# Kernel optimization log

Hardware: AMD Instinct MI355X
Metric: run time of the kernel (lower is better)

Reference implementation:

```python
import jax, jax.numpy as jnp
import numpy as np

N = 8  # fixed node count per sample (hardcoded in the torch module)


def setup_inputs() -> dict:
    key = jax.random.key(0)
    ks = jax.random.split(key, 13)
    B = 131072

    def w(k, shape, fan_in):
        # torch nn.Linear default init: U(-1/sqrt(fan_in), 1/sqrt(fan_in))
        return jax.random.uniform(k, shape, jnp.float32, -1.0, 1.0) / np.sqrt(fan_in).astype(np.float32)

    return {
        "x": jax.random.normal(ks[0], (B, N), jnp.float32),
        "enc_w1": w(ks[1], (3, 64), 3),   "enc_b1": w(ks[2], (64,), 3),
        "enc_w2": w(ks[3], (64, 2), 64),  "enc_b2": w(ks[4], (2,), 64),
        "gcn1_w": w(ks[5], (2, 32), 2),   "gcn1_b": w(ks[6], (32,), 2),
        "gcn2_w": w(ks[7], (32, 32), 32), "gcn2_b": w(ks[8], (32,), 32),
        "dec_w1": w(ks[9], (32, 64), 32), "dec_b1": w(ks[10], (64,), 32),
        "dec_w2": w(ks[11], (64, 3), 64), "dec_b2": w(ks[12], (3,), 64),
    }


def _gabriel_norm_adj(p):
    """Batched Gabriel graph -> GCN-normalized (A + I) with unit edge weights.

    p: (B, N, 2) latent 2D points.
    Edge (i,j) exists iff no other point k lies strictly inside the circle
    with diameter (p_i, p_j)  (dist(p_k, mid)^2 < r^2, matching torch's '<').
    Gabriel graphs contain the nearest-neighbor graph, so for N>=2 edges always
    exist and the torch fallback branch is unreachable.
    Returns D^{-1/2} (A + I) D^{-1/2} of shape (B, N, N) (GCNConv default:
    add_self_loops=True with weight 1, symmetric normalization).
    """
    mid = (p[:, :, None, :] + p[:, None, :, :]) * 0.5                 # (B,N,N,2)
    r2 = jnp.sum((p[:, :, None, :] - mid) ** 2, axis=-1)              # (B,N,N)
    # d2[b,i,j,k] = ||p[b,k] - mid[b,i,j]||^2  -> (B,N,N,N), the big intermediate
    d2 = jnp.sum((p[:, None, None, :, :] - mid[:, :, :, None, :]) ** 2, axis=-1)
    a = jnp.arange(N)
    k_not_ij = (a[None, None, :] != a[:, None, None]) & (a[None, None, :] != a[None, :, None])  # (N,N,N) [i,j,k]
    blocked = jnp.any((d2 < r2[..., None]) & k_not_ij, axis=-1)       # (B,N,N)
    off_diag = a[:, None] != a[None, :]
    adj = ((~blocked) & off_diag).astype(p.dtype)                     # symmetric Gabriel adjacency
    a_hat = adj + jnp.eye(N, dtype=p.dtype)                           # self-loops, weight 1
    dinv = jax.lax.rsqrt(jnp.sum(a_hat, axis=-1))                     # (B,N)
    return dinv[:, :, None] * a_hat * dinv[:, None, :]


def reference(x, enc_w1, enc_b1, enc_w2, enc_b2,
              gcn1_w, gcn1_b, gcn2_w, gcn2_b,
              dec_w1, dec_b1, dec_w2, dec_b2):
    B = x.shape[0]
    idx = jnp.arange(N, dtype=x.dtype)
    # preprocess: (B, N, 3) rows [0, value, index]
    xp = jnp.stack([jnp.zeros_like(x), x, jnp.broadcast_to(idx, x.shape)], axis=-1)
    latent = jax.nn.relu(xp @ enc_w1 + enc_b1) @ enc_w2 + enc_b2      # (B,N,2)
    # torch builds the graph from detach().cpu().numpy() -> no grad through structure
    norm = jax.lax.stop_gradient(_gabriel_norm_adj(latent))           # (B,N,N)
    h1 = jax.nn.relu(jnp.einsum('bij,bjf->bif', norm, latent @ gcn1_w) + gcn1_b)  # (B,N,32)
    h2 = jnp.einsum('bij,bjf->bif', norm, h1 @ gcn2_w) + gcn2_b                    # (B,N,32)
    pooled = jnp.mean(h2, axis=1)                                     # (B,32)
    node = jnp.broadcast_to(pooled[:, None, :], (B, N, pooled.shape[-1]))
    dec = jax.nn.relu(node @ dec_w1 + dec_b1) @ dec_w2 + dec_b2       # (B,N,3)
    reconstructed = dec[:, :, 1]                                      # (B,N)
    return reconstructed, latent
```

## Files before the change

### kernel.cpp

```cpp
#include <hip/hip_runtime.h>


typedef float v2 __attribute__((ext_vector_type(2)));
static __device__ __forceinline__ v2 sp(float s) { return (v2){s, s}; }
static __device__ __forceinline__ v2 fma2(v2 a, v2 b, v2 c) {
    return __builtin_elementwise_fma(a, b, c);
}
static __device__ __forceinline__ v2 ldv2(const float* p) {
    return *reinterpret_cast<const v2*>(p);
}

__global__ __launch_bounds__(256) void gae_aux(
    const float* __restrict__ gcn2_w, const float* __restrict__ gcn2_b,
    const float* __restrict__ dec_w1, const float* __restrict__ dec_b1,
    const float* __restrict__ dec_w2, float* __restrict__ ws)
{
    const int tid = blockIdx.x * 256 + threadIdx.x;
    const int f = tid >> 6, h = tid & 63;
    float acc = 0.0f;
    #pragma unroll 8
    for (int g = 0; g < 32; ++g)
        acc = fmaf(gcn2_w[f * 32 + g], dec_w1[g * 64 + h], acc);
    ws[f * 64 + h] = acc;
    if (tid < 64) {
        float c = dec_b1[h];
        #pragma unroll 8
        for (int g = 0; g < 32; ++g)
            c = fmaf(gcn2_b[g], dec_w1[g * 64 + h], c);
        ws[2048 + h] = c;
        ws[2112 + h] = dec_w2[h * 3 + 1];
    }
}

__global__ __launch_bounds__(256, 4) void gae_main(
    const float* __restrict__ x,
    const float* __restrict__ enc_w1,
    const float* __restrict__ enc_b1,
    const float* __restrict__ enc_w2,
    const float* __restrict__ enc_b2,
    const float* __restrict__ gcn1_w,
    const float* __restrict__ gcn1_b,
    const float* __restrict__ ws,
    const float* __restrict__ dec_b2,
    float* __restrict__ out_rec,
    float* __restrict__ out_lat,
    int B)
{
    __shared__ v2    pbuf[2][8][64];
    __shared__ v2    tbuf[2][16][64];
    __shared__ float obuf[2][2][64];

    const int lane = threadIdx.x & 63;
    const int wid  = threadIdx.x >> 6;
    const int wp   = wid >> 1;
    const int ru   = __builtin_amdgcn_readfirstlane(wid & 1);
    int g = blockIdx.x * 128 + wp * 64 + lane;
    if (g >= B) g = B - 1;

    const float4 xr = *reinterpret_cast<const float4*>(x + (size_t)g * 8 + 4 * ru);
    const v2 xA = (v2){xr.x, xr.y};
    const v2 xB = (v2){xr.z, xr.w};
    const float i0 = (float)(4 * ru);
    const v2 ipA = (v2){i0, i0 + 1.0f};
    const v2 ipB = (v2){i0 + 2.0f, i0 + 3.0f};

    v2 pl0, pl1, pl2, pl3;
    {
        const v2 b2v = ldv2(enc_b2);
        pl0 = b2v; pl1 = b2v; pl2 = b2v; pl3 = b2v;
    }
    #pragma unroll 4
    for (int h = 0; h < 64; ++h) {
        const float wx = enc_w1[64 + h];
        const float wi = enc_w1[128 + h];
        const float bb = enc_b1[h];
        const v2 uxy = ldv2(enc_w2 + 2 * h);
        v2 cA = fma2(ipA, sp(wi), sp(bb));
        v2 cB = fma2(ipB, sp(wi), sp(bb));
        v2 tA = fma2(xA, sp(wx), cA);
        v2 tB = fma2(xB, sp(wx), cB);
        tA = __builtin_elementwise_max(tA, sp(0.0f));
        tB = __builtin_elementwise_max(tB, sp(0.0f));
        pl0 = fma2(sp(tA.x), uxy, pl0);
        pl1 = fma2(sp(tA.y), uxy, pl1);
        pl2 = fma2(sp(tB.x), uxy, pl2);
        pl3 = fma2(sp(tB.y), uxy, pl3);
    }

    {
        float4* lo = reinterpret_cast<float4*>(out_lat + (size_t)g * 16 + 8 * ru);
        lo[0] = make_float4(pl0.x, pl0.y, pl1.x, pl1.y);
        lo[1] = make_float4(pl2.x, pl2.y, pl3.x, pl3.y);
    }

    pbuf[wp][4 * ru + 0][lane] = pl0;
    pbuf[wp][4 * ru + 1][lane] = pl1;
    pbuf[wp][4 * ru + 2][lane] = pl2;
    pbuf[wp][4 * ru + 3][lane] = pl3;
    __syncthreads();
    v2 p[8];
    #pragma unroll
    for (int j = 0; j < 8; ++j) p[j] = pbuf[wp][j][lane];

    unsigned m[8];
    #pragma unroll
    for (int i = 0; i < 8; ++i) m[i] = 1u << i;
    {
        #pragma clang fp contract(off)
        #pragma unroll
        for (int i = 0; i < 8; ++i) {
            #pragma unroll
            for (int j = i + 1; j < 8; ++j) {
                v2 mid = (p[i] + p[j]) * sp(0.5f);
                v2 di = p[i] - mid;  v2 si = di * di;  float r2i = si.x + si.y;
                v2 dj = p[j] - mid;  v2 sj = dj * dj;  float r2j = sj.x + sj.y;
                float dmin = 3.4e38f;
                #pragma unroll
                for (int k = 0; k < 8; ++k) {
                    if (k == i || k == j) continue;
                    v2 dk = p[k] - mid;
                    v2 sk = dk * dk;
                    dmin = fminf(dmin, sk.x + sk.y);
                }
                m[i] |= (dmin < r2i) ? 0u : (1u << j);
                m[j] |= (dmin < r2j) ? 0u : (1u << i);
            }
        }
    }

    float dinv[8];
    #pragma unroll
    for (int i = 0; i < 8; ++i)
        dinv[i] = __builtin_amdgcn_rsqf((float)__popc(m[i]));

    v2 q[8];
    #pragma unroll
    for (int j = 0; j < 8; ++j) q[j] = sp(dinv[j]) * p[j];

    v2 n[8];
    #pragma unroll
    for (int i = 0; i < 8; ++i) {
        v2 acc = sp(0.0f);
        #pragma unroll
        for (int j = 0; j < 8; ++j)
            acc = fma2(sp((float)((m[i] >> j) & 1u)), q[j], acc);
        n[i] = sp(dinv[i]) * acc;
    }

    float cj[8];
    #pragma unroll
    for (int j = 0; j < 8; ++j) {
        float s = 0.0f;
        #pragma unroll
        for (int i = 0; i < 8; ++i)
            s = fmaf((float)((m[i] >> j) & 1u), dinv[i], s);
        cj[j] = 0.125f * dinv[j] * s;
    }

    const float* w0 = gcn1_w + 16 * ru;
    const float* w1 = gcn1_w + 32 + 16 * ru;
    const float* bl = gcn1_b + 16 * ru;
    v2 t2[8];
    #pragma unroll
    for (int fp = 0; fp < 8; ++fp) t2[fp] = sp(0.0f);
    #pragma unroll
    for (int i = 0; i < 8; ++i) {
        const v2 nxi = sp(n[i].x), nyi = sp(n[i].y), ci = sp(cj[i]);
        #pragma unroll
        for (int fp = 0; fp < 8; ++fp) {
            v2 h = fma2(nxi, ldv2(w0 + 2 * fp),
                   fma2(nyi, ldv2(w1 + 2 * fp), ldv2(bl + 2 * fp)));
            h = __builtin_elementwise_max(h, sp(0.0f));
            t2[fp] = fma2(ci, h, t2[fp]);
        }
    }

    #pragma unroll
    for (int fp = 0; fp < 8; ++fp) tbuf[wp][8 * ru + fp][lane] = t2[fp];
    __syncthreads();
    v2 tf[16];
    #pragma unroll
    for (int fp = 0; fp < 16; ++fp) tf[fp] = tbuf[wp][fp][lane];

    const float* Wd = ws + 32 * ru;
    const float* cd = ws + 2048 + 32 * ru;
    const float* w2 = ws + 2112 + 32 * ru;
    v2 a2[16];
    #pragma unroll
    for (int hp = 0; hp < 16; ++hp) a2[hp] = ldv2(cd + 2 * hp);
    #pragma unroll
    for (int f = 0; f < 32; ++f) {
        const v2 pf = sp(tf[f >> 1][f & 1]);
        const float* wr = Wd + f * 64;
        #pragma unroll
        for (int hp = 0; hp < 16; ++hp)
            a2[hp] = fma2(pf, ldv2(wr + 2 * hp), a2[hp]);
    }
    v2 oacc = sp(0.0f);
    #pragma unroll
    for (int hp = 0; hp < 16; ++hp) {
        v2 rr = __builtin_elementwise_max(a2[hp], sp(0.0f));
        oacc = fma2(rr, ldv2(w2 + 2 * hp), oacc);
    }
    const float opart = oacc.x + oacc.y;

    obuf[wp][ru][lane] = opart;
    __syncthreads();
    const float outv = (opart + obuf[wp][1 - ru][lane]) + dec_b2[1];

    {
        float4 r4 = make_float4(outv, outv, outv, outv);
        *reinterpret_cast<float4*>(out_rec + (size_t)g * 8 + 4 * ru) = r4;
    }
}

extern "C" void kernel_launch(void* const* d_in, const int* in_sizes, int n_in,
                              void* d_out, int out_size, void* d_ws, size_t ws_size,
                              hipStream_t stream) {
    const float* x       = (const float*)d_in[0];
    const float* enc_w1  = (const float*)d_in[1];
    const float* enc_b1  = (const float*)d_in[2];
    const float* enc_w2  = (const float*)d_in[3];
    const float* enc_b2  = (const float*)d_in[4];
    const float* gcn1_w  = (const float*)d_in[5];
    const float* gcn1_b  = (const float*)d_in[6];
    const float* gcn2_w  = (const float*)d_in[7];
    const float* gcn2_b  = (const float*)d_in[8];
    const float* dec_w1  = (const float*)d_in[9];
    const float* dec_b1  = (const float*)d_in[10];
    const float* dec_w2  = (const float*)d_in[11];
    const float* dec_b2  = (const float*)d_in[12];

    const int B = in_sizes[0] / 8;
    float* out_rec = (float*)d_out;
    float* out_lat = out_rec + (size_t)B * 8;
    float* ws      = (float*)d_ws;

    gae_aux<<<8, 256, 0, stream>>>(gcn2_w, gcn2_b, dec_w1, dec_b1, dec_w2, ws);

    const int threads = 256;
    const int blocks  = (2 * B + threads - 1) / threads;
    gae_main<<<blocks, threads, 0, stream>>>(
        x, enc_w1, enc_b1, enc_w2, enc_b2,
        gcn1_w, gcn1_b, ws, dec_b2,
        out_rec, out_lat, B);
}
```

Measured before the change: 113.7 us.

## Split each sample across four wavefronts instead of two, sharing graph work

Each sample is now handled by four threads (one per wavefront) instead of two. The 28 Gabriel pair tests are split 7 per wavefront and the adjacency bits are merged through shared memory. The aggregation, GCN and decoder stages are likewise split four ways using shared buffers, and the encoder's index-times-weight-plus-bias term is precomputed into a table by the aux kernel. This cuts per-thread work and register use, allowing 8 waves per SIMD, at the cost of extra barriers and shared-memory traffic.

```diff
diff --git a/kernel.cpp b/kernel.cpp
--- a/kernel.cpp
+++ b/kernel.cpp
@@ -13,7 +13,8 @@
 __global__ __launch_bounds__(256) void gae_aux(
     const float* __restrict__ gcn2_w, const float* __restrict__ gcn2_b,
     const float* __restrict__ dec_w1, const float* __restrict__ dec_b1,
-    const float* __restrict__ dec_w2, float* __restrict__ ws)
+    const float* __restrict__ dec_w2, const float* __restrict__ enc_w1,
+    const float* __restrict__ enc_b1, float* __restrict__ ws)
 {
     const int tid = blockIdx.x * 256 + threadIdx.x;
     const int f = tid >> 6, h = tid & 63;
@@ -30,12 +31,37 @@
         ws[2048 + h] = c;
         ws[2112 + h] = dec_w2[h * 3 + 1];
     }
-}
-
-__global__ __launch_bounds__(256, 4) void gae_main(
+    if (tid < 512) {
+        const int hh = tid >> 3, ii = tid & 7;
+        ws[2176 + tid] = fmaf((float)ii, enc_w1[128 + hh], enc_b1[hh]);
+    }
+}
+
+template <int I, int J>
+static __device__ __forceinline__ void gpair(const v2* __restrict__ p,
+                                             unsigned& ml, unsigned& mh)
+{
+    #pragma clang fp contract(off)
+    v2 mid = (p[I] + p[J]) * sp(0.5f);
+    v2 di = p[I] - mid;  v2 si = di * di;  float r2i = si.x + si.y;
+    v2 dj = p[J] - mid;  v2 sj = dj * dj;  float r2j = sj.x + sj.y;
+    float dmin = 3.4e38f;
+    #pragma unroll
+    for (int k = 0; k < 8; ++k) {
+        if (k == I || k == J) continue;
+        v2 dk = p[k] - mid;
+        v2 sk = dk * dk;
+        dmin = fminf(dmin, sk.x + sk.y);
+    }
+    constexpr unsigned bi = 1u << (((I & 3) * 8) + J);
+    constexpr unsigned bj = 1u << (((J & 3) * 8) + I);
+    if (I < 4) ml |= (dmin < r2i) ? 0u : bi; else mh |= (dmin < r2i) ? 0u : bi;
+    if (J < 4) ml |= (dmin < r2j) ? 0u : bj; else mh |= (dmin < r2j) ? 0u : bj;
+}
+
+__global__ __launch_bounds__(256, 8) void gae_main(
     const float* __restrict__ x,
     const float* __restrict__ enc_w1,
-    const float* __restrict__ enc_b1,
     const float* __restrict__ enc_w2,
     const float* __restrict__ enc_b2,
     const float* __restrict__ gcn1_w,
@@ -46,172 +72,166 @@
     float* __restrict__ out_lat,
     int B)
 {
-    __shared__ v2    pbuf[2][8][64];
-    __shared__ v2    tbuf[2][16][64];
-    __shared__ float obuf[2][2][64];
+    __shared__ union { v2 p[8][64]; v2 t[16][64]; } ptb;
+    __shared__ union { unsigned m[4][2][64]; float o[4][64]; } mob;
+    __shared__ v2    nbuf[8][64];
+    __shared__ float cjbuf[8][64];
 
     const int lane = threadIdx.x & 63;
-    const int wid  = threadIdx.x >> 6;
-    const int wp   = wid >> 1;
-    const int ru   = __builtin_amdgcn_readfirstlane(wid & 1);
-    int g = blockIdx.x * 128 + wp * 64 + lane;
+    const int ru   = __builtin_amdgcn_readfirstlane(threadIdx.x >> 6);
+    int g = blockIdx.x * 64 + lane;
     if (g >= B) g = B - 1;
 
-    const float4 xr = *reinterpret_cast<const float4*>(x + (size_t)g * 8 + 4 * ru);
-    const v2 xA = (v2){xr.x, xr.y};
-    const v2 xB = (v2){xr.z, xr.w};
-    const float i0 = (float)(4 * ru);
-    const v2 ipA = (v2){i0, i0 + 1.0f};
-    const v2 ipB = (v2){i0 + 2.0f, i0 + 3.0f};
-
-    v2 pl0, pl1, pl2, pl3;
-    {
-        const v2 b2v = ldv2(enc_b2);
-        pl0 = b2v; pl1 = b2v; pl2 = b2v; pl3 = b2v;
-    }
-    #pragma unroll 4
+    const float2 xr = *reinterpret_cast<const float2*>(x + (size_t)g * 8 + 2 * ru);
+    const v2 xp2 = (v2){xr.x, xr.y};
+
+    const float* ctab = ws + 2176;
+    v2 pl0, pl1;
+    { const v2 b2v = ldv2(enc_b2); pl0 = b2v; pl1 = b2v; }
+    #pragma unroll 8
     for (int h = 0; h < 64; ++h) {
         const float wx = enc_w1[64 + h];
-        const float wi = enc_w1[128 + h];
-        const float bb = enc_b1[h];
         const v2 uxy = ldv2(enc_w2 + 2 * h);
-        v2 cA = fma2(ipA, sp(wi), sp(bb));
-        v2 cB = fma2(ipB, sp(wi), sp(bb));
-        v2 tA = fma2(xA, sp(wx), cA);
-        v2 tB = fma2(xB, sp(wx), cB);
-        tA = __builtin_elementwise_max(tA, sp(0.0f));
-        tB = __builtin_elementwise_max(tB, sp(0.0f));
-        pl0 = fma2(sp(tA.x), uxy, pl0);
-        pl1 = fma2(sp(tA.y), uxy, pl1);
-        pl2 = fma2(sp(tB.x), uxy, pl2);
-        pl3 = fma2(sp(tB.y), uxy, pl3);
+        const v2 cpr = ldv2(ctab + h * 8 + 2 * ru);
+        v2 t = fma2(xp2, sp(wx), cpr);
+        float t0 = fmaxf(t.x, 0.0f);
+        float t1 = fmaxf(t.y, 0.0f);
+        pl0 = fma2(sp(t0), uxy, pl0);
+        pl1 = fma2(sp(t1), uxy, pl1);
+    }
+
+    *reinterpret_cast<float4*>(out_lat + (size_t)g * 16 + 4 * ru) =
+        make_float4(pl0.x, pl0.y, pl1.x, pl1.y);
+
+    ptb.p[2 * ru + 0][lane] = pl0;
+    ptb.p[2 * ru + 1][lane] = pl1;
+    __syncthreads();
+    v2 p[8];
+    #pragma unroll
+    for (int j = 0; j < 8; ++j) p[j] = ptb.p[j][lane];
+
+    unsigned ml = 0u, mh = 0u;
+    if (ru == 0) {
+        gpair<0,1>(p, ml, mh); gpair<0,2>(p, ml, mh); gpair<0,3>(p, ml, mh);
+        gpair<0,4>(p, ml, mh); gpair<0,5>(p, ml, mh); gpair<0,6>(p, ml, mh);
+        gpair<0,7>(p, ml, mh);
+    } else if (ru == 1) {
+        gpair<1,2>(p, ml, mh); gpair<1,3>(p, ml, mh); gpair<1,4>(p, ml, mh);
+        gpair<1,5>(p, ml, mh); gpair<1,6>(p, ml, mh); gpair<1,7>(p, ml, mh);
+        gpair<2,3>(p, ml, mh);
+    } else if (ru == 2) {
+        gpair<2,4>(p, ml, mh); gpair<2,5>(p, ml, mh); gpair<2,6>(p, ml, mh);
+        gpair<2,7>(p, ml, mh); gpair<3,4>(p, ml, mh); gpair<3,5>(p, ml, mh);
+        gpair<3,6>(p, ml, mh);
+    } else {
+        gpair<3,7>(p, ml, mh); gpair<4,5>(p, ml, mh); gpair<4,6>(p, ml, mh);
+        gpair<4,7>(p, ml, mh); gpair<5,6>(p, ml, mh); gpair<5,7>(p, ml, mh);
+        gpair<6,7>(p, ml, mh);
+    }
+
+    mob.m[ru][0][lane] = ml;
+    mob.m[ru][1][lane] = mh;
+    __syncthreads();
+    ml = (mob.m[0][0][lane] | mob.m[1][0][lane]) |
+         (mob.m[2][0][lane] | mob.m[3][0][lane]) | 0x08040201u;
+    mh = (mob.m[0][1][lane] | mob.m[1][1][lane]) |
+         (mob.m[2][1][lane] | mob.m[3][1][lane]) | 0x80402010u;
+
+    float dinv[8];
+    v2 q[8];
+    #pragma unroll
+    for (int i = 0; i < 8; ++i) {
+        const unsigned rb = ((i < 4 ? ml : mh) >> ((i & 3) * 8)) & 0xffu;
+        dinv[i] = __builtin_amdgcn_rsqf((float)__popc(rb));
+        q[i] = sp(dinv[i]) * p[i];
     }
 
     {
-        float4* lo = reinterpret_cast<float4*>(out_lat + (size_t)g * 16 + 8 * ru);
-        lo[0] = make_float4(pl0.x, pl0.y, pl1.x, pl1.y);
-        lo[1] = make_float4(pl2.x, pl2.y, pl3.x, pl3.y);
-    }
-
-    pbuf[wp][4 * ru + 0][lane] = pl0;
-    pbuf[wp][4 * ru + 1][lane] = pl1;
-    pbuf[wp][4 * ru + 2][lane] = pl2;
-    pbuf[wp][4 * ru + 3][lane] = pl3;
-    __syncthreads();
-    v2 p[8];
-    #pragma unroll
-    for (int j = 0; j < 8; ++j) p[j] = pbuf[wp][j][lane];
-
-    unsigned m[8];
-    #pragma unroll
-    for (int i = 0; i < 8; ++i) m[i] = 1u << i;
-    {
-        #pragma clang fp contract(off)
+        const unsigned w = (ru < 2) ? ml : mh;
+        const int sh = ((2 * ru) & 3) * 8;
+        const unsigned rb0 = (w >> sh) & 0xffu;
+        const unsigned rb1 = (w >> (sh + 8)) & 0xffu;
+        const float dv0 = __builtin_amdgcn_rsqf((float)__popc(rb0));
+        const float dv1 = __builtin_amdgcn_rsqf((float)__popc(rb1));
+        v2 a0 = sp(0.0f), a1 = sp(0.0f);
+        #pragma unroll
+        for (int j = 0; j < 8; ++j) {
+            a0 = fma2(sp((float)((rb0 >> j) & 1u)), q[j], a0);
+            a1 = fma2(sp((float)((rb1 >> j) & 1u)), q[j], a1);
+        }
+        nbuf[2 * ru + 0][lane] = sp(dv0) * a0;
+        nbuf[2 * ru + 1][lane] = sp(dv1) * a1;
+
+        const int j0 = 2 * ru, j1 = 2 * ru + 1;
+        float s0 = 0.0f, s1 = 0.0f;
         #pragma unroll
         for (int i = 0; i < 8; ++i) {
-            #pragma unroll
-            for (int j = i + 1; j < 8; ++j) {
-                v2 mid = (p[i] + p[j]) * sp(0.5f);
-                v2 di = p[i] - mid;  v2 si = di * di;  float r2i = si.x + si.y;
-                v2 dj = p[j] - mid;  v2 sj = dj * dj;  float r2j = sj.x + sj.y;
-                float dmin = 3.4e38f;
-                #pragma unroll
-                for (int k = 0; k < 8; ++k) {
-                    if (k == i || k == j) continue;
-                    v2 dk = p[k] - mid;
-                    v2 sk = dk * dk;
-                    dmin = fminf(dmin, sk.x + sk.y);
-                }
-                m[i] |= (dmin < r2i) ? 0u : (1u << j);
-                m[j] |= (dmin < r2j) ? 0u : (1u << i);
-            }
-        }
-    }
-
-    float dinv[8];
-    #pragma unroll
-    for (int i = 0; i < 8; ++i)
-        dinv[i] = __builtin_amdgcn_rsqf((float)__popc(m[i]));
-
-    v2 q[8];
-    #pragma unroll
-    for (int j = 0; j < 8; ++j) q[j] = sp(dinv[j]) * p[j];
-
-    v2 n[8];
+            const unsigned rb = ((i < 4 ? ml : mh) >> ((i & 3) * 8)) & 0xffu;
+            s0 = fmaf((float)((rb >> j0) & 1u), dinv[i], s0);
+            s1 = fmaf((float)((rb >> j1) & 1u), dinv[i], s1);
+        }
+        cjbuf[j0][lane] = 0.125f * dv0 * s0;
+        cjbuf[j1][lane] = 0.125f * dv1 * s1;
+    }
+    __syncthreads();
+
+    const float* w0 = gcn1_w + 8 * ru;
+    const float* w1 = gcn1_w + 32 + 8 * ru;
+    const float* bl = gcn1_b + 8 * ru;
+    v2 t2[4];
+    #pragma unroll
+    for (int fp = 0; fp < 4; ++fp) t2[fp] = sp(0.0f);
     #pragma unroll
     for (int i = 0; i < 8; ++i) {
-        v2 acc = sp(0.0f);
-        #pragma unroll
-        for (int j = 0; j < 8; ++j)
-            acc = fma2(sp((float)((m[i] >> j) & 1u)), q[j], acc);
-        n[i] = sp(dinv[i]) * acc;
-    }
-
-    float cj[8];
-    #pragma unroll
-    for (int j = 0; j < 8; ++j) {
-        float s = 0.0f;
-        #pragma unroll
-        for (int i = 0; i < 8; ++i)
-            s = fmaf((float)((m[i] >> j) & 1u), dinv[i], s);
-        cj[j] = 0.125f * dinv[j] * s;
-    }
-
-    const float* w0 = gcn1_w + 16 * ru;
-    const float* w1 = gcn1_w + 32 + 16 * ru;
-    const float* bl = gcn1_b + 16 * ru;
-    v2 t2[8];
-    #pragma unroll
-    for (int fp = 0; fp < 8; ++fp) t2[fp] = sp(0.0f);
-    #pragma unroll
-    for (int i = 0; i < 8; ++i) {
-        const v2 nxi = sp(n[i].x), nyi = sp(n[i].y), ci = sp(cj[i]);
-        #pragma unroll
-        for (int fp = 0; fp < 8; ++fp) {
+        const v2 ni = nbuf[i][lane];
+        const float ci = cjbuf[i][lane];
+        const v2 nxi = sp(ni.x), nyi = sp(ni.y), civ = sp(ci);
+        #pragma unroll
+        for (int fp = 0; fp < 4; ++fp) {
             v2 h = fma2(nxi, ldv2(w0 + 2 * fp),
                    fma2(nyi, ldv2(w1 + 2 * fp), ldv2(bl + 2 * fp)));
             h = __builtin_elementwise_max(h, sp(0.0f));
-            t2[fp] = fma2(ci, h, t2[fp]);
-        }
-    }
-
-    #pragma unroll
-    for (int fp = 0; fp < 8; ++fp) tbuf[wp][8 * ru + fp][lane] = t2[fp];
-    __syncthreads();
-    v2 tf[16];
-    #pragma unroll
-    for (int fp = 0; fp < 16; ++fp) tf[fp] = tbuf[wp][fp][lane];
-
-    const float* Wd = ws + 32 * ru;
-    const float* cd = ws + 2048 + 32 * ru;
-    const float* w2 = ws + 2112 + 32 * ru;
-    v2 a2[16];
-    #pragma unroll
-    for (int hp = 0; hp < 16; ++hp) a2[hp] = ldv2(cd + 2 * hp);
-    #pragma unroll
-    for (int f = 0; f < 32; ++f) {
-        const v2 pf = sp(tf[f >> 1][f & 1]);
-        const float* wr = Wd + f * 64;
-        #pragma unroll
-        for (int hp = 0; hp < 16; ++hp)
-            a2[hp] = fma2(pf, ldv2(wr + 2 * hp), a2[hp]);
+            t2[fp] = fma2(civ, h, t2[fp]);
+        }
+    }
+
+    #pragma unroll
+    for (int fp = 0; fp < 4; ++fp) ptb.t[4 * ru + fp][lane] = t2[fp];
+    __syncthreads();
+
+    const float* Wd = ws + 16 * ru;
+    const float* cd = ws + 2048 + 16 * ru;
+    const float* w2 = ws + 2112 + 16 * ru;
+    v2 a2[8];
+    #pragma unroll
+    for (int hp = 0; hp < 8; ++hp) a2[hp] = ldv2(cd + 2 * hp);
+    #pragma unroll
+    for (int fp = 0; fp < 16; ++fp) {
+        const v2 tv = ptb.t[fp][lane];
+        const float* wrA = Wd + (2 * fp) * 64;
+        const float* wrB = Wd + (2 * fp + 1) * 64;
+        const v2 tA = sp(tv.x), tB = sp(tv.y);
+        #pragma unroll
+        for (int hp = 0; hp < 8; ++hp) {
+            a2[hp] = fma2(tA, ldv2(wrA + 2 * hp), a2[hp]);
+            a2[hp] = fma2(tB, ldv2(wrB + 2 * hp), a2[hp]);
+        }
     }
     v2 oacc = sp(0.0f);
     #pragma unroll
-    for (int hp = 0; hp < 16; ++hp) {
+    for (int hp = 0; hp < 8; ++hp) {
         v2 rr = __builtin_elementwise_max(a2[hp], sp(0.0f));
         oacc = fma2(rr, ldv2(w2 + 2 * hp), oacc);
     }
     const float opart = oacc.x + oacc.y;
 
-    obuf[wp][ru][lane] = opart;
-    __syncthreads();
-    const float outv = (opart + obuf[wp][1 - ru][lane]) + dec_b2[1];
-
-    {
-        float4 r4 = make_float4(outv, outv, outv, outv);
-        *reinterpret_cast<float4*>(out_rec + (size_t)g * 8 + 4 * ru) = r4;
-    }
+    mob.o[ru][lane] = opart;
+    __syncthreads();
+    const float outv = ((mob.o[0][lane] + mob.o[1][lane]) +
+                        (mob.o[2][lane] + mob.o[3][lane])) + dec_b2[1];
+
+    *reinterpret_cast<float2*>(out_rec + (size_t)g * 8 + 2 * ru) =
+        make_float2(outv, outv);
 }
 
 extern "C" void kernel_launch(void* const* d_in, const int* in_sizes, int n_in,
@@ -236,12 +256,12 @@
     float* out_lat = out_rec + (size_t)B * 8;
     float* ws      = (float*)d_ws;
 
-    gae_aux<<<8, 256, 0, stream>>>(gcn2_w, gcn2_b, dec_w1, dec_b1, dec_w2, ws);
-
-    const int threads = 256;
-    const int blocks  = (2 * B + threads - 1) / threads;
-    gae_main<<<blocks, threads, 0, stream>>>(
-        x, enc_w1, enc_b1, enc_w2, enc_b2,
+    gae_aux<<<8, 256, 0, stream>>>(gcn2_w, gcn2_b, dec_w1, dec_b1, dec_w2,
+                                   enc_w1, enc_b1, ws);
+
+    const int blocks = (B + 63) / 64;
+    gae_main<<<blocks, 256, 0, stream>>>(
+        x, enc_w1, enc_w2, enc_b2,
         gcn1_w, gcn1_b, ws, dec_b2,
         out_rec, out_lat, B);
 }
```

After: 107.0 us. 5.8% less time.
